# Kernel tuning notes

Measured on AMD Instinct MI355X. Metric: run time of the kernel, lower is better.

Reference implementation:

```python
import jax, jax.numpy as jnp
from jax import lax
import numpy as np


def setup_inputs() -> dict:
    key = jax.random.key(0)
    ks = jax.random.split(key, 7)
    T, B, I, H = 512, 64, 1024, 1024
    std = 1.0 / np.sqrt(H)
    u = lambda k, shape: jax.random.uniform(k, shape, jnp.float32, -std, std)
    return {
        "x": jax.random.normal(ks[0], (T, B, I), jnp.float32),
        "h0": jax.random.normal(ks[1], (B, H), jnp.float32),
        "c0": jax.random.normal(ks[2], (B, H), jnp.float32),
        "w_ih": u(ks[3], (4 * H, I)),
        "w_hh": u(ks[4], (4 * H, H)),
        "b_ih": u(ks[5], (4 * H,)),
        "b_hh": u(ks[6], (4 * H,)),
    }


def reference(x, h0, c0, w_ih, w_hh, b_ih, b_hh):
    # Precompute input projection for all timesteps in one big GEMM:
    # [T, B, 4H]. Biases folded in (b_ih + b_hh, as in the torch code).
    xg = jnp.einsum("tbi,gi->tbg", x, w_ih) + (b_ih + b_hh)

    def step(carry, xg_t):
        h, c = carry
        gates = xg_t + h @ w_hh.T  # [B, 4H]
        i_g, f_g, g_g, o_g = jnp.split(gates, 4, axis=-1)
        c = jax.nn.sigmoid(f_g) * c + jax.nn.sigmoid(i_g) * jnp.tanh(g_g)
        h = jax.nn.sigmoid(o_g) * jnp.tanh(c)
        return (h, c), None

    (h, c), _ = lax.scan(step, (h0, c0), xg)
    return (h, c)
```

## Files before the change

kernel.cpp:

```cpp
#include <hip/hip_runtime.h>
#include <hip/hip_bf16.h>
#include <stdint.h>


typedef short  short8 __attribute__((ext_vector_type(8)));
typedef float  f32x4  __attribute__((ext_vector_type(4)));
typedef int    i32x4  __attribute__((ext_vector_type(4)));

#define T_STEPS 512

__device__ __forceinline__ unsigned short f2bf(float f) {
    uint32_t u = __float_as_uint(f);
    return (unsigned short)((u + 0x7fffu + ((u >> 16) & 1u)) >> 16);
}
__device__ __forceinline__ float bf2f(unsigned short v) {
    return __uint_as_float(((uint32_t)v) << 16);
}
__device__ __forceinline__ float sigf(float x)  { return 1.0f / (1.0f + __expf(-x)); }
__device__ __forceinline__ float tanhf_(float x){ return 1.0f - 2.0f / (__expf(2.0f * x) + 1.0f); }

__device__ __forceinline__ i32x4 load16_agent(const void* p) {
    i32x4 r;
    asm volatile("global_load_dwordx4 %0, %1, off sc0 sc1"
                 : "=v"(r) : "v"(p) : "memory");
    return r;
}

__global__ void k_setup(const float* __restrict__ w_ih,
                        const float* __restrict__ b_ih, const float* __restrict__ b_hh,
                        const float* __restrict__ h0,
                        unsigned short* __restrict__ wb, float* __restrict__ bias,
                        unsigned short* __restrict__ hb0, unsigned* __restrict__ flags) {
    int idx = blockIdx.x * blockDim.x + threadIdx.x;
    int stride = gridDim.x * blockDim.x;
    const float4* w4 = (const float4*)w_ih;
    ushort4* wb4 = (ushort4*)wb;
    for (int i = idx; i < 1048576; i += stride) {
        float4 v = w4[i];
        wb4[i] = make_ushort4(f2bf(v.x), f2bf(v.y), f2bf(v.z), f2bf(v.w));
    }
    const float4* bi4 = (const float4*)b_ih;
    const float4* bh4 = (const float4*)b_hh;
    float4* bs4 = (float4*)bias;
    for (int i = idx; i < 1024; i += stride) {
        float4 a = bi4[i], b = bh4[i];
        bs4[i] = make_float4(a.x + b.x, a.y + b.y, a.z + b.z, a.w + b.w);
    }
    const float4* h04 = (const float4*)h0;
    ushort4* hb4 = (ushort4*)hb0;
    for (int i = idx; i < 16384; i += stride) {
        float4 v = h04[i];
        hb4[i] = make_ushort4(f2bf(v.x), f2bf(v.y), f2bf(v.z), f2bf(v.w));
    }
    for (int i = idx; i < 131072; i += stride) flags[i] = 0u;
}

__device__ __forceinline__ short8 lds_frag(const unsigned short* base, int row, int kbyte) {
    unsigned off = (unsigned)(row * 128 + kbyte);
    off ^= (unsigned)((row & 7) << 4);
    return *(const short8*)((const char*)base + off);
}

__global__ __launch_bounds__(256) void k_gemm(const float* __restrict__ x,
                                              const unsigned short* __restrict__ wb,
                                              const float* __restrict__ bias,
                                              unsigned short* __restrict__ xg) {
    __shared__ __align__(16) unsigned short As[128 * 64];
    __shared__ __align__(16) unsigned short Bs[128 * 64];
    unsigned orig = blockIdx.x;
    unsigned xcd = orig & 7, idx = orig >> 3;
    unsigned n_t = xcd * 4 + (idx >> 8);
    unsigned m_t = idx & 255;
    const int m0 = (int)m_t * 128, n0 = (int)n_t * 128;
    const int tid = threadIdx.x;
    const int lane = tid & 63, w = tid >> 6;
    const int wr = w >> 1, wc = w & 1;
    const int r = lane & 15, kq = lane >> 4;

    f32x4 acc[4][4] = {};

    const int ar = tid >> 1, ah = tid & 1;

    for (int k0 = 0; k0 < 1024; k0 += 64) {
        {
            const float4* src = (const float4*)(x + (size_t)(m0 + ar) * 1024 + k0 + ah * 32);
            unsigned aw_base = (unsigned)(ar * 128 + ah * 64);
            unsigned sw = (unsigned)((ar & 7) << 4);
            #pragma unroll
            for (int i = 0; i < 4; ++i) {
                float4 v0 = src[2 * i], v1 = src[2 * i + 1];
                short8 p;
                p[0] = (short)f2bf(v0.x); p[1] = (short)f2bf(v0.y);
                p[2] = (short)f2bf(v0.z); p[3] = (short)f2bf(v0.w);
                p[4] = (short)f2bf(v1.x); p[5] = (short)f2bf(v1.y);
                p[6] = (short)f2bf(v1.z); p[7] = (short)f2bf(v1.w);
                *(short8*)((char*)As + ((aw_base + i * 16) ^ sw)) = p;
            }
        }
        {
            const short8* src = (const short8*)(wb + (size_t)(n0 + ar) * 1024 + k0 + ah * 32);
            unsigned bw_base = (unsigned)(ar * 128 + ah * 64);
            unsigned sw = (unsigned)((ar & 7) << 4);
            #pragma unroll
            for (int i = 0; i < 4; ++i) {
                short8 p = src[i];
                *(short8*)((char*)Bs + ((bw_base + i * 16) ^ sw)) = p;
            }
        }
        __syncthreads();
        #pragma unroll
        for (int kk = 0; kk < 2; ++kk) {
            short8 af[4], bfr[4];
            #pragma unroll
            for (int i = 0; i < 4; ++i) af[i]  = lds_frag(As, wr * 64 + i * 16 + r, (kk * 32 + kq * 8) * 2);
            #pragma unroll
            for (int j = 0; j < 4; ++j) bfr[j] = lds_frag(Bs, wc * 64 + j * 16 + r, (kk * 32 + kq * 8) * 2);
            #pragma unroll
            for (int i = 0; i < 4; ++i)
                #pragma unroll
                for (int j = 0; j < 4; ++j)
                    acc[i][j] = __builtin_amdgcn_mfma_f32_16x16x32_bf16(af[i], bfr[j], acc[i][j], 0, 0, 0);
        }
        __syncthreads();
    }

    const int t_idx = (m0 + wr * 64) >> 6;
    const size_t tb = (size_t)t_idx * 256;
    #pragma unroll
    for (int j = 0; j < 4; ++j) {
        int nn = n0 + wc * 64 + j * 16 + r;
        float bsum = bias[nn];
        int g = nn >> 10, jj = nn & 1023;
        int jgx = jj >> 4, jlx = jj & 15;
        #pragma unroll
        for (int i = 0; i < 4; ++i) {
            size_t off = ((tb + (size_t)i * 64 + jgx) * 4 + g) * 256 + (size_t)(kq * 4) * 16 + jlx;
            #pragma unroll
            for (int q = 0; q < 4; ++q)
                xg[off + (size_t)q * 16] = f2bf(acc[i][j][q] + bsum);
        }
    }
}

__global__ __launch_bounds__(256, 1) void k_lstm(
    const float* __restrict__ w_hh, const float* __restrict__ c0g,
    const unsigned short* __restrict__ xg,
    unsigned short* __restrict__ hbuf,
    unsigned* __restrict__ flags,
    float* __restrict__ outH, float* __restrict__ outC) {
    __shared__ __align__(16) unsigned short h_lds[16 * 1024];
    __shared__ float g_lds[4 * 256];

    const unsigned L = blockIdx.x;
    const unsigned bg = L >> 6, jg = L & 63;
    const int tid = threadIdx.x, lane = tid & 63, w = tid >> 6;
    const int r = lane & 15, kq = lane >> 4;

    const int n = (w << 10) + (int)jg * 16 + r;
    short8 bfrag[32];
    {
        const float4* wrow = (const float4*)(w_hh + (size_t)n * 1024 + kq * 8);
        #pragma unroll
        for (int kit = 0; kit < 32; ++kit) {
            float4 v0 = wrow[kit * 8];
            float4 v1 = wrow[kit * 8 + 1];
            short8 p;
            p[0] = (short)f2bf(v0.x); p[1] = (short)f2bf(v0.y);
            p[2] = (short)f2bf(v0.z); p[3] = (short)f2bf(v0.w);
            p[4] = (short)f2bf(v1.x); p[5] = (short)f2bf(v1.y);
            p[6] = (short)f2bf(v1.z); p[7] = (short)f2bf(v1.w);
            bfrag[kit] = p;
        }
    }

    const int bl = tid >> 3, jp = tid & 7;
    const size_t cellIdx = (size_t)(bg * 16 + (bl & 15)) * 1024 + jg * 16 + jp * 2;
    float c0r = 0.f, c1r = 0.f;
    if (tid < 128) { c0r = c0g[cellIdx]; c1r = c0g[cellIdx + 1]; }

    for (int t = 0; t < T_STEPS; ++t) {
        const unsigned short* hp = hbuf + (size_t)(t & 1) * 65536;
        unsigned short* hn = hbuf + (size_t)((t + 1) & 1) * 65536;

        if (t > 0 && w == 0) {
            const unsigned* fl = flags + ((unsigned)(t - 1) * 4u + bg) * 64u;
            while (true) {
                unsigned f = __hip_atomic_load(fl + lane, __ATOMIC_RELAXED,
                                               __HIP_MEMORY_SCOPE_AGENT);
                if (__ballot(f != 0u) == ~0ull) break;
                __builtin_amdgcn_s_sleep(1);
            }
        }
        __syncthreads();

        {
            const char* src = (const char*)(hp + (size_t)bg * 16 * 1024);
            i32x4 stg[8];
            #pragma unroll
            for (int i = 0; i < 8; ++i)
                stg[i] = load16_agent(src + (unsigned)tid * 16u + (unsigned)i * 4096u);
            asm volatile("s_waitcnt vmcnt(0)" ::: "memory");
            __builtin_amdgcn_sched_barrier(0);
            #pragma unroll
            for (int i = 0; i < 8; ++i) {
                unsigned off = (unsigned)tid * 16u + (unsigned)i * 4096u;
                unsigned row = off >> 11, colb = off & 2047u;
                *(i32x4*)((char*)h_lds + row * 2048u + (colb ^ ((row & 7u) << 4))) = stg[i];
            }
        }
        __syncthreads();

        const unsigned short* xgp = xg + (((size_t)t * 256 + L) * 4 + w) * 256;
        float xv[4];
        #pragma unroll
        for (int q = 0; q < 4; ++q) xv[q] = bf2f(xgp[(kq * 4 + q) * 16 + r]);

        f32x4 acc0 = {0.f, 0.f, 0.f, 0.f}, acc1 = {0.f, 0.f, 0.f, 0.f};
        const char* arow = (const char*)h_lds + (unsigned)r * 2048u;
        const unsigned asw = ((unsigned)(r & 7)) << 4;
        #pragma unroll
        for (int kit = 0; kit < 32; kit += 2) {
            short8 a0 = *(const short8*)(arow + (((unsigned)kit * 64u + (unsigned)kq * 16u) ^ asw));
            short8 a1 = *(const short8*)(arow + (((unsigned)(kit + 1) * 64u + (unsigned)kq * 16u) ^ asw));
            acc0 = __builtin_amdgcn_mfma_f32_16x16x32_bf16(a0, bfrag[kit], acc0, 0, 0, 0);
            acc1 = __builtin_amdgcn_mfma_f32_16x16x32_bf16(a1, bfrag[kit + 1], acc1, 0, 0, 0);
        }
        f32x4 acc = acc0 + acc1;
        #pragma unroll
        for (int q = 0; q < 4; ++q)
            g_lds[w * 256 + (kq * 4 + q) * 16 + r] = acc[q] + xv[q];
        __syncthreads();

        if (tid < 128) {
            int gb = (bl & 15) * 16 + jp * 2;
            float gi0 = g_lds[gb],       gi1 = g_lds[gb + 1];
            float gf0 = g_lds[256 + gb], gf1 = g_lds[256 + gb + 1];
            float gg0 = g_lds[512 + gb], gg1 = g_lds[512 + gb + 1];
            float go0 = g_lds[768 + gb], go1 = g_lds[768 + gb + 1];
            c0r = sigf(gf0) * c0r + sigf(gi0) * tanhf_(gg0);
            c1r = sigf(gf1) * c1r + sigf(gi1) * tanhf_(gg1);
            float h0v = sigf(go0) * tanhf_(c0r);
            float h1v = sigf(go1) * tanhf_(c1r);
            unsigned packed = (unsigned)f2bf(h0v) | ((unsigned)f2bf(h1v) << 16);
            __hip_atomic_store((unsigned*)(hn + cellIdx), packed,
                               __ATOMIC_RELAXED, __HIP_MEMORY_SCOPE_AGENT);
            if (t == T_STEPS - 1) {
                outH[cellIdx] = h0v; outH[cellIdx + 1] = h1v;
                outC[cellIdx] = c0r; outC[cellIdx + 1] = c1r;
            }
        }
        asm volatile("s_waitcnt vmcnt(0)" ::: "memory");
        __syncthreads();
        if (tid == 0)
            __hip_atomic_store(flags + ((unsigned)t * 4u + bg) * 64u + jg, 1u,
                               __ATOMIC_RELAXED, __HIP_MEMORY_SCOPE_AGENT);
    }
}

extern "C" void kernel_launch(void* const* d_in, const int* in_sizes, int n_in,
                              void* d_out, int out_size, void* d_ws, size_t ws_size,
                              hipStream_t stream) {
    const float* x    = (const float*)d_in[0];
    const float* h0   = (const float*)d_in[1];
    const float* c0   = (const float*)d_in[2];
    const float* w_ih = (const float*)d_in[3];
    const float* w_hh = (const float*)d_in[4];
    const float* b_ih = (const float*)d_in[5];
    const float* b_hh = (const float*)d_in[6];

    float* outH = (float*)d_out;
    float* outC = outH + 65536;

    uint8_t* ws = (uint8_t*)d_ws;
    unsigned short* xg    = (unsigned short*)ws;
    unsigned short* wb    = (unsigned short*)(ws + 268435456ULL);
    float*          bias  = (float*)(ws + 276824064ULL);
    unsigned short* hbuf  = (unsigned short*)(ws + 276840448ULL);
    unsigned*       flags = (unsigned*)(ws + 277102592ULL);

    k_setup<<<1024, 256, 0, stream>>>(w_ih, b_ih, b_hh, h0, wb, bias, hbuf, flags);
    k_gemm<<<8192, 256, 0, stream>>>(x, wb, bias, xg);
    k_lstm<<<256, 256, 0, stream>>>(w_hh, c0, xg, hbuf, flags, outH, outC);
}
```

Measured before the change: 3.612 ms.

## Restructure LSTM recurrence into single-wave blocks with monotonic counter flags

```diff
diff --git a/kernel.cpp b/kernel.cpp
--- a/kernel.cpp
+++ b/kernel.cpp
@@ -18,13 +18,6 @@
 }
 __device__ __forceinline__ float sigf(float x)  { return 1.0f / (1.0f + __expf(-x)); }
 __device__ __forceinline__ float tanhf_(float x){ return 1.0f - 2.0f / (__expf(2.0f * x) + 1.0f); }
-
-__device__ __forceinline__ i32x4 load16_agent(const void* p) {
-    i32x4 r;
-    asm volatile("global_load_dwordx4 %0, %1, off sc0 sc1"
-                 : "=v"(r) : "v"(p) : "memory");
-    return r;
-}
 
 __global__ void k_setup(const float* __restrict__ w_ih,
                         const float* __restrict__ b_ih, const float* __restrict__ b_hh,
@@ -52,7 +45,7 @@
         float4 v = h04[i];
         hb4[i] = make_ushort4(f2bf(v.x), f2bf(v.y), f2bf(v.z), f2bf(v.w));
     }
-    for (int i = idx; i < 131072; i += stride) flags[i] = 0u;
+    for (int i = idx; i < 512; i += stride) flags[i] = 0u;
 }
 
 __device__ __forceinline__ short8 lds_frag(const unsigned short* base, int row, int kbyte) {
@@ -124,137 +117,158 @@
         __syncthreads();
     }
 
-    const int t_idx = (m0 + wr * 64) >> 6;
-    const size_t tb = (size_t)t_idx * 256;
+    const int t_idx = (int)m_t * 2 + wr;
     #pragma unroll
     for (int j = 0; j < 4; ++j) {
         int nn = n0 + wc * 64 + j * 16 + r;
         float bsum = bias[nn];
-        int g = nn >> 10, jj = nn & 1023;
-        int jgx = jj >> 4, jlx = jj & 15;
+        int gate = nn >> 10, jcol = nn & 1023;
+        int jgc = jcol >> 4, jloc = jcol & 15;
+        int wvc = jloc >> 3, p = (jloc >> 2) & 1, jlc = jloc & 3;
+        int lane_c = kq * 16 + gate * 4 + jlc;
         #pragma unroll
         for (int i = 0; i < 4; ++i) {
-            size_t off = ((tb + (size_t)i * 64 + jgx) * 4 + g) * 256 + (size_t)(kq * 4) * 16 + jlx;
+            size_t base = ((((size_t)t_idx * 4 + i) * 64 + jgc) * 2 + wvc) * 512
+                          + (size_t)lane_c * 8 + p * 4;
             #pragma unroll
             for (int q = 0; q < 4; ++q)
-                xg[off + (size_t)q * 16] = f2bf(acc[i][j][q] + bsum);
-        }
-    }
-}
-
-__global__ __launch_bounds__(256, 1) void k_lstm(
+                xg[base + q] = f2bf(acc[i][j][q] + bsum);
+        }
+    }
+}
+
+#define LA(OFF) asm volatile("global_load_dwordx4 %0, %1, off offset:" #OFF " sc0 sc1" \
+                             : "=v"(a[(OFF)/64]) : "v"(ap) : "memory")
+
+__global__ __launch_bounds__(64, 1) void k_lstm(
     const float* __restrict__ w_hh, const float* __restrict__ c0g,
     const unsigned short* __restrict__ xg,
     unsigned short* __restrict__ hbuf,
     unsigned* __restrict__ flags,
     float* __restrict__ outH, float* __restrict__ outC) {
-    __shared__ __align__(16) unsigned short h_lds[16 * 1024];
-    __shared__ float g_lds[4 * 256];
+    __shared__ float gx[2][16][4][4];
 
     const unsigned L = blockIdx.x;
-    const unsigned bg = L >> 6, jg = L & 63;
-    const int tid = threadIdx.x, lane = tid & 63, w = tid >> 6;
+    const unsigned bg = L >> 7, widx = L & 127;
+    const unsigned jg = widx >> 1, wv = widx & 1;
+    const int lane = threadIdx.x & 63;
     const int r = lane & 15, kq = lane >> 4;
-
-    const int n = (w << 10) + (int)jg * 16 + r;
-    short8 bfrag[32];
+    const int lg = r >> 2, jl = r & 3;
+
+    short8 bf0[32], bf1[32];
     {
-        const float4* wrow = (const float4*)(w_hh + (size_t)n * 1024 + kq * 8);
+        const int n0 = lg * 1024 + (int)(jg * 16 + wv * 8) + jl;
+        const float4* w0p = (const float4*)(w_hh + (size_t)n0 * 1024 + kq * 8);
+        const float4* w1p = (const float4*)(w_hh + (size_t)(n0 + 4) * 1024 + kq * 8);
         #pragma unroll
         for (int kit = 0; kit < 32; ++kit) {
-            float4 v0 = wrow[kit * 8];
-            float4 v1 = wrow[kit * 8 + 1];
+            float4 v0 = w0p[kit * 8], v1 = w0p[kit * 8 + 1];
             short8 p;
             p[0] = (short)f2bf(v0.x); p[1] = (short)f2bf(v0.y);
             p[2] = (short)f2bf(v0.z); p[3] = (short)f2bf(v0.w);
             p[4] = (short)f2bf(v1.x); p[5] = (short)f2bf(v1.y);
             p[6] = (short)f2bf(v1.z); p[7] = (short)f2bf(v1.w);
-            bfrag[kit] = p;
-        }
-    }
-
-    const int bl = tid >> 3, jp = tid & 7;
-    const size_t cellIdx = (size_t)(bg * 16 + (bl & 15)) * 1024 + jg * 16 + jp * 2;
-    float c0r = 0.f, c1r = 0.f;
-    if (tid < 128) { c0r = c0g[cellIdx]; c1r = c0g[cellIdx + 1]; }
+            bf0[kit] = p;
+            float4 u0 = w1p[kit * 8], u1 = w1p[kit * 8 + 1];
+            short8 qv;
+            qv[0] = (short)f2bf(u0.x); qv[1] = (short)f2bf(u0.y);
+            qv[2] = (short)f2bf(u0.z); qv[3] = (short)f2bf(u0.w);
+            qv[4] = (short)f2bf(u1.x); qv[5] = (short)f2bf(u1.y);
+            qv[6] = (short)f2bf(u1.z); qv[7] = (short)f2bf(u1.w);
+            bf1[kit] = qv;
+        }
+    }
+
+    const int grow = (int)bg * 16 + kq * 4 + lg;
+    const int col0 = (int)(jg * 16 + wv * 8) + jl;
+    const size_t o0 = (size_t)grow * 1024 + col0;
+    float c0r = c0g[o0], c1r = c0g[o0 + 4];
+    float h0v = 0.f, h1v = 0.f;
+
+    const unsigned arow_off = (unsigned)(((int)bg * 16 + r) * 1024 + kq * 8) * 2u;
+    const unsigned* fl = flags + bg * 128u;
+    unsigned* myflag = flags + bg * 128u + widx;
 
     for (int t = 0; t < T_STEPS; ++t) {
-        const unsigned short* hp = hbuf + (size_t)(t & 1) * 65536;
-        unsigned short* hn = hbuf + (size_t)((t + 1) & 1) * 65536;
-
-        if (t > 0 && w == 0) {
-            const unsigned* fl = flags + ((unsigned)(t - 1) * 4u + bg) * 64u;
+        if (t > 0) {
+            const unsigned tt = (unsigned)t;
             while (true) {
-                unsigned f = __hip_atomic_load(fl + lane, __ATOMIC_RELAXED,
-                                               __HIP_MEMORY_SCOPE_AGENT);
-                if (__ballot(f != 0u) == ~0ull) break;
-                __builtin_amdgcn_s_sleep(1);
+                unsigned p0 = __hip_atomic_load(fl + lane, __ATOMIC_RELAXED,
+                                                __HIP_MEMORY_SCOPE_AGENT);
+                unsigned p1 = __hip_atomic_load(fl + 64 + lane, __ATOMIC_RELAXED,
+                                                __HIP_MEMORY_SCOPE_AGENT);
+                if (__ballot((p0 >= tt) && (p1 >= tt)) == ~0ull) break;
+                __builtin_amdgcn_s_sleep(2);
             }
         }
-        __syncthreads();
-
-        {
-            const char* src = (const char*)(hp + (size_t)bg * 16 * 1024);
-            i32x4 stg[8];
-            #pragma unroll
-            for (int i = 0; i < 8; ++i)
-                stg[i] = load16_agent(src + (unsigned)tid * 16u + (unsigned)i * 4096u);
+
+        const char* ap = (const char*)(hbuf + (size_t)(t & 1) * 65536) + arow_off;
+        i32x4 a[32];
+        LA(0);    LA(64);   LA(128);  LA(192);  LA(256);  LA(320);  LA(384);  LA(448);
+        LA(512);  LA(576);  LA(640);  LA(704);  LA(768);  LA(832);  LA(896);  LA(960);
+        LA(1024); LA(1088); LA(1152); LA(1216); LA(1280); LA(1344); LA(1408); LA(1472);
+        LA(1536); LA(1600); LA(1664); LA(1728); LA(1792); LA(1856); LA(1920); LA(1984);
+        short8 xv = *(const short8*)(xg + ((((size_t)t * 4 + bg) * 64 + jg) * 2 + wv) * 512
+                                     + (size_t)lane * 8);
+        asm volatile("s_waitcnt vmcnt(1)" ::: "memory");
+        __builtin_amdgcn_sched_barrier(0);
+
+        f32x4 ae0 = {0.f,0.f,0.f,0.f}, ao0 = {0.f,0.f,0.f,0.f};
+        f32x4 ae1 = {0.f,0.f,0.f,0.f}, ao1 = {0.f,0.f,0.f,0.f};
+        #pragma unroll
+        for (int kit = 0; kit < 32; kit += 2) {
+            short8 av0 = __builtin_bit_cast(short8, a[kit]);
+            short8 av1 = __builtin_bit_cast(short8, a[kit + 1]);
+            ae0 = __builtin_amdgcn_mfma_f32_16x16x32_bf16(av0, bf0[kit], ae0, 0, 0, 0);
+            ae1 = __builtin_amdgcn_mfma_f32_16x16x32_bf16(av0, bf1[kit], ae1, 0, 0, 0);
+            ao0 = __builtin_amdgcn_mfma_f32_16x16x32_bf16(av1, bf0[kit + 1], ao0, 0, 0, 0);
+            ao1 = __builtin_amdgcn_mfma_f32_16x16x32_bf16(av1, bf1[kit + 1], ao1, 0, 0, 0);
+        }
+        asm volatile("s_waitcnt vmcnt(0)" ::: "memory");
+        __builtin_amdgcn_sched_barrier(0);
+        f32x4 acc0 = ae0 + ao0, acc1 = ae1 + ao1;
+        #pragma unroll
+        for (int q = 0; q < 4; ++q) {
+            acc0[q] += bf2f((unsigned short)xv[q]);
+            acc1[q] += bf2f((unsigned short)xv[4 + q]);
+        }
+
+        #pragma unroll
+        for (int q = 0; q < 4; ++q) {
+            gx[0][kq * 4 + q][lg][jl] = acc0[q];
+            gx[1][kq * 4 + q][lg][jl] = acc1[q];
+        }
+        __builtin_amdgcn_sched_barrier(0);
+        const int rs = kq * 4 + lg;
+        float i0 = gx[0][rs][0][jl], fz0 = gx[0][rs][1][jl];
+        float g0 = gx[0][rs][2][jl], oz0 = gx[0][rs][3][jl];
+        float i1 = gx[1][rs][0][jl], fz1 = gx[1][rs][1][jl];
+        float g1 = gx[1][rs][2][jl], oz1 = gx[1][rs][3][jl];
+
+        c0r = sigf(fz0) * c0r + sigf(i0) * tanhf_(g0);
+        h0v = sigf(oz0) * tanhf_(c0r);
+        c1r = sigf(fz1) * c1r + sigf(i1) * tanhf_(g1);
+        h1v = sigf(oz1) * tanhf_(c1r);
+
+        if (t < T_STEPS - 1) {
+            unsigned short* hn = hbuf + (size_t)((t + 1) & 1) * 65536;
+            unsigned hv0 = f2bf(h0v), hv1 = f2bf(h1v);
+            unsigned short* s0p = hn + o0;
+            unsigned short* s1p = s0p + 4;
+            asm volatile("global_store_short %0, %1, off sc0 sc1"
+                         :: "v"(s0p), "v"(hv0) : "memory");
+            asm volatile("global_store_short %0, %1, off sc0 sc1"
+                         :: "v"(s1p), "v"(hv1) : "memory");
             asm volatile("s_waitcnt vmcnt(0)" ::: "memory");
             __builtin_amdgcn_sched_barrier(0);
-            #pragma unroll
-            for (int i = 0; i < 8; ++i) {
-                unsigned off = (unsigned)tid * 16u + (unsigned)i * 4096u;
-                unsigned row = off >> 11, colb = off & 2047u;
-                *(i32x4*)((char*)h_lds + row * 2048u + (colb ^ ((row & 7u) << 4))) = stg[i];
-            }
-        }
-        __syncthreads();
-
-        const unsigned short* xgp = xg + (((size_t)t * 256 + L) * 4 + w) * 256;
-        float xv[4];
-        #pragma unroll
-        for (int q = 0; q < 4; ++q) xv[q] = bf2f(xgp[(kq * 4 + q) * 16 + r]);
-
-        f32x4 acc0 = {0.f, 0.f, 0.f, 0.f}, acc1 = {0.f, 0.f, 0.f, 0.f};
-        const char* arow = (const char*)h_lds + (unsigned)r * 2048u;
-        const unsigned asw = ((unsigned)(r & 7)) << 4;
-        #pragma unroll
-        for (int kit = 0; kit < 32; kit += 2) {
-            short8 a0 = *(const short8*)(arow + (((unsigned)kit * 64u + (unsigned)kq * 16u) ^ asw));
-            short8 a1 = *(const short8*)(arow + (((unsigned)(kit + 1) * 64u + (unsigned)kq * 16u) ^ asw));
-            acc0 = __builtin_amdgcn_mfma_f32_16x16x32_bf16(a0, bfrag[kit], acc0, 0, 0, 0);
-            acc1 = __builtin_amdgcn_mfma_f32_16x16x32_bf16(a1, bfrag[kit + 1], acc1, 0, 0, 0);
-        }
-        f32x4 acc = acc0 + acc1;
-        #pragma unroll
-        for (int q = 0; q < 4; ++q)
-            g_lds[w * 256 + (kq * 4 + q) * 16 + r] = acc[q] + xv[q];
-        __syncthreads();
-
-        if (tid < 128) {
-            int gb = (bl & 15) * 16 + jp * 2;
-            float gi0 = g_lds[gb],       gi1 = g_lds[gb + 1];
-            float gf0 = g_lds[256 + gb], gf1 = g_lds[256 + gb + 1];
-            float gg0 = g_lds[512 + gb], gg1 = g_lds[512 + gb + 1];
-            float go0 = g_lds[768 + gb], go1 = g_lds[768 + gb + 1];
-            c0r = sigf(gf0) * c0r + sigf(gi0) * tanhf_(gg0);
-            c1r = sigf(gf1) * c1r + sigf(gi1) * tanhf_(gg1);
-            float h0v = sigf(go0) * tanhf_(c0r);
-            float h1v = sigf(go1) * tanhf_(c1r);
-            unsigned packed = (unsigned)f2bf(h0v) | ((unsigned)f2bf(h1v) << 16);
-            __hip_atomic_store((unsigned*)(hn + cellIdx), packed,
-                               __ATOMIC_RELAXED, __HIP_MEMORY_SCOPE_AGENT);
-            if (t == T_STEPS - 1) {
-                outH[cellIdx] = h0v; outH[cellIdx + 1] = h1v;
-                outC[cellIdx] = c0r; outC[cellIdx + 1] = c1r;
-            }
-        }
-        asm volatile("s_waitcnt vmcnt(0)" ::: "memory");
-        __syncthreads();
-        if (tid == 0)
-            __hip_atomic_store(flags + ((unsigned)t * 4u + bg) * 64u + jg, 1u,
-                               __ATOMIC_RELAXED, __HIP_MEMORY_SCOPE_AGENT);
-    }
+            if (lane == 0)
+                __hip_atomic_store(myflag, (unsigned)(t + 1),
+                                   __ATOMIC_RELAXED, __HIP_MEMORY_SCOPE_AGENT);
+        }
+    }
+
+    outH[o0] = h0v; outH[o0 + 4] = h1v;
+    outC[o0] = c0r; outC[o0 + 4] = c1r;
 }
 
 extern "C" void kernel_launch(void* const* d_in, const int* in_sizes, int n_in,
@@ -280,5 +294,5 @@
 
     k_setup<<<1024, 256, 0, stream>>>(w_ih, b_ih, b_hh, h0, wb, bias, hbuf, flags);
     k_gemm<<<8192, 256, 0, stream>>>(x, wb, bias, xg);
-    k_lstm<<<256, 256, 0, stream>>>(w_hh, c0, xg, hbuf, flags, outH, outC);
-}
+    k_lstm<<<512, 64, 0, stream>>>(w_hh, c0, xg, hbuf, flags, outH, outC);
+}
```

Measured after the change: 5.434 ms. 50.4% more time.
